# Performance work log

Hardware: AMD Instinct MI355X
Metric: run time of the kernel (lower is better)

Reference implementation:

```python
import jax, jax.numpy as jnp
import numpy as np

S, B, V, E, H = 64, 32, 32000, 512, 1024


def gru_cell(x, h, Wih, Whh, bih, bhh):
    # PyTorch GRU cell math. x: [B, in], h: [B, H]
    gi = x @ Wih.T + bih          # [B, 3H]
    gh = h @ Whh.T + bhh          # [B, 3H]
    ir, iz, inn = jnp.split(gi, 3, axis=-1)
    hr, hz, hn = jnp.split(gh, 3, axis=-1)
    r = jax.nn.sigmoid(ir + hr)
    z = jax.nn.sigmoid(iz + hz)
    n = jnp.tanh(inn + r * hn)
    return (1.0 - z) * n + z * h


def run_gru(xs, h0, Wih, Whh, bih, bhh):
    def step(h, x):
        h = gru_cell(x, h, Wih, Whh, bih, bhh)
        return h, h
    _, hs = jax.lax.scan(step, h0, xs)
    return hs  # [S, B, H]


def setup_inputs():
    key = jax.random.key(0)
    ks = jax.random.split(key, 24)
    n = lambda k, shp, s=0.05: (jax.random.normal(k, shp, jnp.float32) * s)
    inp = {
        "input_seq": jax.random.randint(ks[0], (S, B), 0, V),
        "target_seq": jax.random.randint(ks[1], (S, B), 0, V),
        "emb": n(ks[2], (V, E)),
        # bidirectional encoder GRU (forward / backward directions)
        "enc_Wih_f": n(ks[3], (3 * H, E)), "enc_Whh_f": n(ks[4], (3 * H, H)),
        "enc_bih_f": n(ks[5], (3 * H,)),  "enc_bhh_f": n(ks[6], (3 * H,)),
        "enc_Wih_b": n(ks[7], (3 * H, E)), "enc_Whh_b": n(ks[8], (3 * H, H)),
        "enc_bih_b": n(ks[9], (3 * H,)),  "enc_bhh_b": n(ks[10], (3 * H,)),
        "encoder_init": n(ks[11], (2, H), 0.1),
        # decoder GRU: input = token(E) + glimpse(2H) + last_output(E)
        "dec_Wih": n(ks[12], (3 * H, 2 * E + 2 * H)), "dec_Whh": n(ks[13], (3 * H, H)),
        "dec_bih": n(ks[14], (3 * H,)), "dec_bhh": n(ks[15], (3 * H,)),
        "dec_init_h": n(ks[16], (H,), 0.1),
        "dec_init_out": n(ks[17], (E,), 0.1),
        "attn_W1": n(ks[18], (H, 3 * H)),  # Linear(3H -> H, bias=False)
        "attn_W2": n(ks[19], (1, H)),      # Linear(H -> 1, bias=False)
        "out_W": n(ks[20], (V, H)), "out_b": n(ks[21], (V,)),
    }
    return inp


def reference(input_seq, target_seq, emb,
              enc_Wih_f, enc_Whh_f, enc_bih_f, enc_bhh_f,
              enc_Wih_b, enc_Whh_b, enc_bih_b, enc_bhh_b, encoder_init,
              dec_Wih, dec_Whh, dec_bih, dec_bhh, dec_init_h, dec_init_out,
              attn_W1, attn_W2, out_W, out_b):
    x = emb[input_seq]            # [S, B, E]
    tgt = emb[target_seq]         # [S, B, E]
    bsz = x.shape[1]

    # bidirectional encoder
    h0f = jnp.broadcast_to(encoder_init[0], (bsz, H))
    h0b = jnp.broadcast_to(encoder_init[1], (bsz, H))
    fwd = run_gru(x, h0f, enc_Wih_f, enc_Whh_f, enc_bih_f, enc_bhh_f)
    bwd = run_gru(x[::-1], h0b, enc_Wih_b, enc_Whh_b, enc_bih_b, enc_bhh_b)[::-1]
    enc = jnp.concatenate([fwd, bwd], axis=-1)  # [S, B, 2H]

    def step(carry, inp_t):
        h, last_out = carry                      # [B,H], [B,E]
        tok, tg = inp_t                          # [B,E], [B,E]
        hexp = jnp.broadcast_to(h[None], (S, bsz, H))
        a = jnp.concatenate([enc, hexp], axis=-1)            # [S, B, 3H]
        scores = jnp.tanh(a @ attn_W1.T) @ attn_W2.T          # [S, B, 1]
        # NOTE: original uses nn.Softmax(dim=1) on [S,B,1] -> softmax over BATCH dim
        w = jax.nn.softmax(scores, axis=1)
        glimpse = (enc * w).sum(axis=0)                       # [B, 2H]
        dec_in = jnp.concatenate([tok, glimpse, last_out], axis=-1)
        h = gru_cell(dec_in, h, dec_Wih, dec_Whh, dec_bih, dec_bhh)
        probs = jax.nn.softmax(h @ out_W.T + out_b, axis=1)   # [B, V]
        return (h, tg), probs

    h0 = jnp.broadcast_to(dec_init_h, (bsz, H))
    o0 = jnp.broadcast_to(dec_init_out, (bsz, E))
    _, outs = jax.lax.scan(step, (h0, o0), (x, tgt))
    return outs  # [S, B, V]
```

## Files before the change

kernel.cpp:

```cpp
#include <hip/hip_runtime.h>
#include <hip/hip_bf16.h>

#define S_ 64
#define B_ 32
#define V_ 32000
#define E_ 512
#define H_ 1024
#define H3_ 3072

typedef __hip_bfloat16 bf16;
typedef __attribute__((ext_vector_type(8))) short s8v;
typedef __attribute__((ext_vector_type(4))) float f4;
typedef unsigned long long ull;

__device__ __forceinline__ float b2f(bf16 x){ return __bfloat162float(x); }
__device__ __forceinline__ bf16  f2b(float x){ return __float2bfloat16(x); }
__device__ __forceinline__ float bfu2f(unsigned short u){
  union { unsigned u; float f; } c; c.u = ((unsigned)u) << 16; return c.f;
}
#define MFMA16(a,b,c) __builtin_amdgcn_mfma_f32_16x16x32_bf16((a),(b),(c),0,0,0)

__device__ __forceinline__ float fsigmoid(float x){ return 1.f/(1.f + __expf(-x)); }
__device__ __forceinline__ float ftanh(float x){ float e2 = __expf(2.f*x); return 1.f - 2.f/(e2 + 1.f); }

__global__ __launch_bounds__(256) void cast_bf16_k(const float* __restrict__ s, bf16* __restrict__ d, int n8){
  int stride = gridDim.x*256;
  for (int i = blockIdx.x*256 + threadIdx.x; i < n8; i += stride){
    f4 a = *((const f4*)s + (size_t)i*2);
    f4 b = *((const f4*)s + (size_t)i*2 + 1);
    union { s8v v; bf16 h[8]; } o;
    #pragma unroll
    for (int k=0;k<4;k++){ o.h[k]=f2b(a[k]); o.h[4+k]=f2b(b[k]); }
    *((s8v*)d + i) = o.v;
  }
}
__global__ __launch_bounds__(256) void cast2_k(const float* __restrict__ s0, const float* __restrict__ s1,
                                               bf16* __restrict__ d0, bf16* __restrict__ d1, int n8){
  const float* s = blockIdx.y ? s1 : s0;
  bf16* d = blockIdx.y ? d1 : d0;
  int stride = gridDim.x*256;
  for (int i = blockIdx.x*256 + threadIdx.x; i < n8; i += stride){
    f4 a = *((const f4*)s + (size_t)i*2);
    f4 b = *((const f4*)s + (size_t)i*2 + 1);
    union { s8v v; bf16 h[8]; } o;
    #pragma unroll
    for (int k=0;k<4;k++){ o.h[k]=f2b(a[k]); o.h[4+k]=f2b(b[k]); }
    *((s8v*)d + i) = o.v;
  }
}
__global__ __launch_bounds__(256) void cast4_k(const float* __restrict__ s0, const float* __restrict__ s1,
                                               const float* __restrict__ s2, const float* __restrict__ s3,
                                               bf16* __restrict__ d0, bf16* __restrict__ d1,
                                               bf16* __restrict__ d2, bf16* __restrict__ d3, int n8){
  const float* s = (blockIdx.y==0)?s0:(blockIdx.y==1)?s1:(blockIdx.y==2)?s2:s3;
  bf16* d = (blockIdx.y==0)?d0:(blockIdx.y==1)?d1:(blockIdx.y==2)?d2:d3;
  int stride = gridDim.x*256;
  for (int i = blockIdx.x*256 + threadIdx.x; i < n8; i += stride){
    f4 a = *((const f4*)s + (size_t)i*2);
    f4 b = *((const f4*)s + (size_t)i*2 + 1);
    union { s8v v; bf16 h[8]; } o;
    #pragma unroll
    for (int k=0;k<4;k++){ o.h[k]=f2b(a[k]); o.h[4+k]=f2b(b[k]); }
    *((s8v*)d + i) = o.v;
  }
}
__global__ __launch_bounds__(256) void gather_x_k(const float* __restrict__ emb, const int* __restrict__ seq, bf16* __restrict__ d){
  int i = blockIdx.x*256 + threadIdx.x;
  int row = i >> 6, e8 = i & 63;
  const float* src = emb + (size_t)seq[row]*E_;
  f4 a = *((const f4*)src + e8*2);
  f4 b = *((const f4*)src + e8*2 + 1);
  union { s8v v; bf16 h[8]; } o;
  #pragma unroll
  for (int k=0;k<4;k++){ o.h[k]=f2b(a[k]); o.h[4+k]=f2b(b[k]); }
  *((s8v*)d + i) = o.v;
}
__global__ __launch_bounds__(256) void gather_lo_k(const float* __restrict__ emb, const int* __restrict__ tseq, const float* __restrict__ o0, bf16* __restrict__ d){
  int i = blockIdx.x*256 + threadIdx.x;
  int row = i >> 6, e8 = i & 63;
  int t = row >> 5, b = row & 31;
  const float* src = (t == 0) ? o0 : (emb + (size_t)tseq[(t-1)*B_ + b]*E_);
  f4 a = *((const f4*)src + e8*2);
  f4 c = *((const f4*)src + e8*2 + 1);
  union { s8v v; bf16 h[8]; } o;
  #pragma unroll
  for (int k=0;k<4;k++){ o.h[k]=f2b(a[k]); o.h[4+k]=f2b(c[k]); }
  *((s8v*)d + i) = o.v;
}

template<int WB16, int ACC>
__global__ __launch_bounds__(256) void gemm_bt(const bf16* __restrict__ A, int lda,
                                               const bf16* __restrict__ B, int ldb,
                                               const float* __restrict__ bias,
                                               void* __restrict__ Cp, int ldc, int K)
{
  __shared__ bf16 a_sm[128][40];
  __shared__ bf16 b_sm[128][40];
  const int tid = threadIdx.x;
  const int m0 = blockIdx.y*128, n0 = blockIdx.x*128;
  const int w = tid>>6, l = tid&63;
  const int wm = w>>1, wn = w&1;
  f4 acc[4][4];
  #pragma unroll
  for (int i=0;i<4;i++)
    #pragma unroll
    for (int j=0;j<4;j++) acc[i][j] = (f4){0.f,0.f,0.f,0.f};
  const int srow = tid>>1, skc = (tid&1)*16;
  const int ar = l&15, koff = (l>>4)*8;
  for (int k0 = 0; k0 < K; k0 += 32){
    __syncthreads();
    const s8v* pa = (const s8v*)(A + (size_t)(m0+srow)*lda + k0 + skc);
    const s8v* pb = (const s8v*)(B + (size_t)(n0+srow)*ldb + k0 + skc);
    *(s8v*)&a_sm[srow][skc]   = pa[0];
    *(s8v*)&a_sm[srow][skc+8] = pa[1];
    *(s8v*)&b_sm[srow][skc]   = pb[0];
    *(s8v*)&b_sm[srow][skc+8] = pb[1];
    __syncthreads();
    s8v av[4], bv[4];
    #pragma unroll
    for (int i=0;i<4;i++) av[i] = *(const s8v*)&a_sm[wm*64 + i*16 + ar][koff];
    #pragma unroll
    for (int j=0;j<4;j++) bv[j] = *(const s8v*)&b_sm[wn*64 + j*16 + ar][koff];
    #pragma unroll
    for (int i=0;i<4;i++)
      #pragma unroll
      for (int j=0;j<4;j++)
        acc[i][j] = MFMA16(av[i], bv[j], acc[i][j]);
  }
  const int rb = (l>>4)*4;
  #pragma unroll
  for (int i=0;i<4;i++){
    #pragma unroll
    for (int j=0;j<4;j++){
      int col = n0 + wn*64 + j*16 + ar;
      float badd = bias ? bias[col] : 0.f;
      #pragma unroll
      for (int r=0;r<4;r++){
        int row = m0 + wm*64 + i*16 + rb + r;
        size_t idx = (size_t)row*ldc + col;
        float v = acc[i][j][r] + badd;
        if (ACC) v += ((const float*)Cp)[idx];
        if (WB16) ((bf16*)Cp)[idx] = f2b(v);
        else      ((float*)Cp)[idx] = v;
      }
    }
  }
}

__global__ __launch_bounds__(256) void enc_init_k(const float* __restrict__ enc_init,
                                                  const float* __restrict__ bihf, const float* __restrict__ bihb,
                                                  bf16* __restrict__ hb0, float* __restrict__ hfE,
                                                  float* __restrict__ bias_fb){
  int i = blockIdx.x*256 + threadIdx.x;
  int base = i*8;
  int dir = base>>15, rem = base&32767, col = rem&1023;
  const float* sp = enc_init + dir*H_ + col;
  f4 a = *(const f4*)sp, b = *(const f4*)(sp+4);
  union { s8v v; bf16 h[8]; } o;
  #pragma unroll
  for (int k=0;k<4;k++){ o.h[k]=f2b(a[k]); o.h[4+k]=f2b(b[k]); }
  *(s8v*)(hb0 + dir*32768 + rem) = o.v;
  *(f4*)(hfE + dir*32768 + rem) = a;
  *(f4*)(hfE + dir*32768 + rem + 4) = b;
  if (i < 6144) bias_fb[i] = (i < 3072) ? bihf[i] : bihb[i-3072];
}
__global__ __launch_bounds__(256) void dec_init_k(const float* __restrict__ dinh,
                                                  bf16* __restrict__ hd0, float* __restrict__ hfD){
  int i = blockIdx.x*256 + threadIdx.x;
  int base = i*8;
  int col = base&1023;
  const float* sp = dinh + col;
  f4 a = *(const f4*)sp, b = *(const f4*)(sp+4);
  union { s8v v; bf16 h[8]; } o;
  #pragma unroll
  for (int k=0;k<4;k++){ o.h[k]=f2b(a[k]); o.h[4+k]=f2b(b[k]); }
  *(s8v*)(hd0 + base) = o.v;
  *(f4*)(hfD + base) = a;
  *(f4*)(hfD + base + 4) = b;
}

__global__ __launch_bounds__(256) void enc_step_k(
  const float* __restrict__ gi_fb,
  const bf16* __restrict__ whhf, const bf16* __restrict__ whhb,
  const float* __restrict__ bhhf, const float* __restrict__ bhhb,
  const bf16* __restrict__ hrd_base, bf16* __restrict__ hwr_base,
  float* __restrict__ hfE, bf16* __restrict__ enc_out, int s)
{
  __shared__ bf16 hst[16][1032];
  __shared__ bf16 hsT[16][64];
  const int tid = threadIdx.x, bid = blockIdx.x;
  const int w = tid>>6, l = tid&63;
  const int lr = l&15, koff = (l>>4)*8, rb = (l>>4)*4;
  const int x = bid&7, g3 = bid>>3;
  const int dir = x>>2;
  const int mt = g3>>2;
  const int jtb = (x&3)*16 + (g3&3)*4;
  const int jt = jtb + w;
  const int col = jt*16 + lr;
  const bf16* W    = dir ? whhb : whhf;
  const float* bhh = dir ? bhhb : bhhf;
  const float br_ = bhh[col], bz_ = bhh[H_+col], bn_ = bhh[2*H_+col];
  const bf16* pr = W + (size_t)(jt*16 + lr)*H_ + koff;
  const bf16* pz = pr + (size_t)H_*H_;
  const bf16* pn = pz + (size_t)H_*H_;
  {
    const bf16* src = hrd_base + dir*32768 + (size_t)mt*16*H_;
    #pragma unroll
    for (int c = 0; c < 8; ++c){
      int g = c*256 + tid;
      int row = g>>7, off = g&127;
      *(s8v*)&hst[row][off*8] = *(const s8v*)(src + (size_t)row*H_ + off*8);
    }
  }
  __syncthreads();
  f4 accr = (f4){0,0,0,0}, accz = (f4){0,0,0,0}, accn = (f4){0,0,0,0};
  #pragma unroll 4
  for (int k0 = 0; k0 < H_; k0 += 32){
    s8v a = *(const s8v*)&hst[lr][koff + k0];
    accr = MFMA16(a, *(const s8v*)(pr + k0), accr);
    accz = MFMA16(a, *(const s8v*)(pz + k0), accz);
    accn = MFMA16(a, *(const s8v*)(pn + k0), accn);
  }
  const int es = dir ? (63 - s) : s;
  const int dcol = dir*3072 + col;
  #pragma unroll
  for (int ri = 0; ri < 4; ++ri){
    const int b_ = mt*16 + rb + ri;
    const size_t gr = (size_t)(es*B_ + b_)*6144;
    float ir = gi_fb[gr + dcol], iz = gi_fb[gr + 1024 + dcol], inn = gi_fb[gr + 2048 + dcol];
    float rg = fsigmoid(ir + accr[ri] + br_);
    float zg = fsigmoid(iz + accz[ri] + bz_);
    float ng = ftanh(inn + rg*(accn[ri] + bn_));
    float hold = hfE[dir*32768 + b_*H_ + col];
    float hnew = (1.f - zg)*ng + zg*hold;
    hfE[dir*32768 + b_*H_ + col] = hnew;
    hsT[rb+ri][w*16+lr] = f2b(hnew);
  }
  __syncthreads();
  {
    const int row = tid>>4, seg = tid&15;
    ull v = *(ull*)&hsT[row][seg*4];
    *(ull*)(hwr_base + dir*32768 + (size_t)(mt*16+row)*H_ + jtb*16 + seg*4) = v;
    *(ull*)(enc_out + (size_t)(es*B_ + mt*16+row)*2048 + dir*H_ + jtb*16 + seg*4) = v;
  }
}

__global__ __launch_bounds__(256) void dec_kA(
  const bf16* __restrict__ hd,
  const bf16* __restrict__ whhd, const float* __restrict__ bhhd,
  const bf16* __restrict__ w1b,
  const bf16* __restrict__ encW1b,
  const float* __restrict__ attnW2,
  float* __restrict__ gh,
  float* __restrict__ sc4)
{
  __shared__ bf16 hst[16][1032];
  __shared__ float ghT[16][128];
  __shared__ bf16 hbst[1024];
  __shared__ float hw1s[256];
  const int tid = threadIdx.x, bid = blockIdx.x;
  const int w = tid>>6, l = tid&63;
  const int lr = l&15, koff = (l>>4)*8;
  if (bid < 48){
    const int gmt = bid&1;
    const int rest = bid>>1;
    const int x3 = rest/3, gkk = rest%3;
    const int ntb = x3*24 + gkk*8;
    {
      const bf16* src = hd + (size_t)gmt*16*H_;
      #pragma unroll
      for (int c = 0; c < 8; ++c){
        int g = c*256 + tid;
        int row = g>>7, off = g&127;
        *(s8v*)&hst[row][off*8] = *(const s8v*)(src + (size_t)row*H_ + off*8);
      }
    }
    __syncthreads();
    #pragma unroll
    for (int q = 0; q < 2; ++q){
      const int nt = ntb + w*2 + q;
      const bf16* pb = whhd + (size_t)(nt*16 + lr)*H_ + koff;
      const float bv = bhhd[nt*16 + lr];
      f4 acc = (f4){0,0,0,0};
      #pragma unroll 4
      for (int k0 = 0; k0 < H_; k0 += 32)
        acc = MFMA16(*(const s8v*)&hst[lr][koff+k0], *(const s8v*)(pb+k0), acc);
      #pragma unroll
      for (int r = 0; r < 4; ++r)
        ghT[(l>>4)*4+r][(w*2+q)*16 + lr] = acc[r] + bv;
    }
    __syncthreads();
    #pragma unroll
    for (int i = 0; i < 4; ++i){
      int idx = tid + i*256;
      int row = idx>>6, seg = idx&63;
      union{ float f[2]; ull u; } pk;
      pk.f[0] = ghT[row][seg*2]; pk.f[1] = ghT[row][seg*2+1];
      *(ull*)(gh + (size_t)(gmt*16+row)*H3_ + ntb*16 + seg*2) = pk.u;
    }
  } else {
    const int idx = bid - 48;
    const int b = idx>>2, q = idx&3;
    if (tid < 128) *(s8v*)&hbst[tid*8] = *(const s8v*)(hd + (size_t)b*H_ + tid*8);
    __syncthreads();
    const bf16* pb0 = w1b + (size_t)(q*256 + (w*4+0)*16 + lr)*H3_ + 2048 + koff;
    const bf16* pb1 = w1b + (size_t)(q*256 + (w*4+1)*16 + lr)*H3_ + 2048 + koff;
    const bf16* pb2 = w1b + (size_t)(q*256 + (w*4+2)*16 + lr)*H3_ + 2048 + koff;
    const bf16* pb3 = w1b + (size_t)(q*256 + (w*4+3)*16 + lr)*H3_ + 2048 + koff;
    f4 a0 = (f4){0,0,0,0}, a1 = (f4){0,0,0,0}, a2 = (f4){0,0,0,0}, a3 = (f4){0,0,0,0};
    #pragma unroll 4
    for (int k0 = 0; k0 < H_; k0 += 32){
      s8v a = *(const s8v*)&hbst[koff + k0];
      a0 = MFMA16(a, *(const s8v*)(pb0 + k0), a0);
      a1 = MFMA16(a, *(const s8v*)(pb1 + k0), a1);
      a2 = MFMA16(a, *(const s8v*)(pb2 + k0), a2);
      a3 = MFMA16(a, *(const s8v*)(pb3 + k0), a3);
    }
    if (l < 16){
      hw1s[(w*4+0)*16 + l] = a0[0];
      hw1s[(w*4+1)*16 + l] = a1[0];
      hw1s[(w*4+2)*16 + l] = a2[0];
      hw1s[(w*4+3)*16 + l] = a3[0];
    }
    __syncthreads();
    const int s = tid>>2, part = tid&3;
    const bf16* ep = encW1b + ((size_t)s*B_ + b)*H_ + q*256 + part*64;
    const float* w2p = attnW2 + q*256 + part*64;
    const float* hp = hw1s + part*64;
    float p = 0.f;
    #pragma unroll 2
    for (int ii = 0; ii < 8; ++ii){
      union { s8v v; unsigned short uu[8]; } ev;
      ev.v = *(const s8v*)(ep + ii*8);
      f4 wa = *(const f4*)(w2p + ii*8);
      f4 wb = *(const f4*)(w2p + ii*8 + 4);
      #pragma unroll
      for (int k = 0; k < 8; ++k){
        float xx = bfu2f(ev.uu[k]) + hp[ii*8+k];
        p += (k<4 ? wa[k] : wb[k-4])*ftanh(xx);
      }
    }
    p += __shfl_xor(p,1); p += __shfl_xor(p,2);
    if (part == 0) sc4[q*2048 + s*32 + b] = p;
  }
}

__global__ __launch_bounds__(256) void dec_kB(
  const float* __restrict__ gi_t,
  const bf16* __restrict__ encWgb, const float* __restrict__ gh,
  const float* __restrict__ sc4,
  float* __restrict__ hfD, bf16* __restrict__ hd_w, bf16* __restrict__ hall_t)
{
  __shared__ float watst[64];
  __shared__ float part_[4][3][256];
  __shared__ bf16 hnewst[256];
  const int tid = threadIdx.x, bid = blockIdx.x;
  const int x = bid&7, g3 = bid>>3;
  const int db = 4*x + (g3&3), jq = g3>>2;
  const int jD = jq*256 + tid;
  if (tid < 64){
    const int s = tid;
    f4 v[8];
    #pragma unroll
    for (int c = 0; c < 8; ++c) v[c] = *(const f4*)(sc4 + s*32 + c*4);
    #pragma unroll
    for (int q = 1; q < 4; ++q)
      #pragma unroll
      for (int c = 0; c < 8; ++c) v[c] += *(const f4*)(sc4 + q*2048 + s*32 + c*4);
    float m = -1e30f;
    #pragma unroll
    for (int c = 0; c < 8; ++c)
      #pragma unroll
      for (int k = 0; k < 4; ++k) m = fmaxf(m, v[c][k]);
    float Z = 0.f;
    #pragma unroll
    for (int c = 0; c < 8; ++c)
      #pragma unroll
      for (int k = 0; k < 4; ++k) Z += __expf(v[c][k] - m);
    watst[s] = __expf(v[db>>2][db&3] - m)/Z;
  }
  __syncthreads();
  const int lane = tid&63, wv = tid>>6;
  const int j0 = jq*256 + lane*4;
  f4 g0 = (f4){0,0,0,0}, g1 = (f4){0,0,0,0}, g2 = (f4){0,0,0,0};
  #pragma unroll 4
  for (int i = 0; i < 16; ++i){
    const int s2 = wv*16 + i;
    const float wt = watst[s2];
    const bf16* ro = encWgb + ((size_t)s2*B_ + db)*H3_;
    union{ ull u; unsigned short us[4]; } v0, v1, v2;
    v0.u = *(const ull*)(ro + j0);
    v1.u = *(const ull*)(ro + H_ + j0);
    v2.u = *(const ull*)(ro + 2*H_ + j0);
    #pragma unroll
    for (int k = 0; k < 4; ++k){
      g0[k] += wt*bfu2f(v0.us[k]);
      g1[k] += wt*bfu2f(v1.us[k]);
      g2[k] += wt*bfu2f(v2.us[k]);
    }
  }
  *(f4*)&part_[wv][0][lane*4] = g0;
  *(f4*)&part_[wv][1][lane*4] = g1;
  *(f4*)&part_[wv][2][lane*4] = g2;
  __syncthreads();
  float G0 = part_[0][0][tid]+part_[1][0][tid]+part_[2][0][tid]+part_[3][0][tid];
  float G1 = part_[0][1][tid]+part_[1][1][tid]+part_[2][1][tid]+part_[3][1][tid];
  float G2 = part_[0][2][tid]+part_[1][2][tid]+part_[2][2][tid]+part_[3][2][tid];
  const float* gp = gi_t + (size_t)db*H3_ + jD;
  float ir  = gp[0]    + G0;
  float iz  = gp[H_]   + G1;
  float inn = gp[2*H_] + G2;
  float hr_ = gh[(size_t)db*H3_ + jD];
  float hz_ = gh[(size_t)db*H3_ + H_ + jD];
  float hn_ = gh[(size_t)db*H3_ + 2*H_ + jD];
  float rg = fsigmoid(ir + hr_);
  float zg = fsigmoid(iz + hz_);
  float ng = ftanh(inn + rg*hn_);
  float hold = hfD[(size_t)db*H_ + jD];
  float hnew = (1.f - zg)*ng + zg*hold;
  hfD[(size_t)db*H_ + jD] = hnew;
  hnewst[tid] = f2b(hnew);
  __syncthreads();
  if (tid < 64){
    ull v = *(ull*)&hnewst[tid*4];
    *(ull*)(hd_w + (size_t)db*H_ + jq*256 + tid*4) = v;
    *(ull*)(hall_t + (size_t)db*H_ + jq*256 + tid*4) = v;
  }
}

__global__ __launch_bounds__(256) void softmax_rows_k(float* __restrict__ out){
  __shared__ float wm[4], wl[4];
  const int tid = threadIdx.x;
  float* p = out + (size_t)blockIdx.x*V_;
  float m = -1e30f, lsum = 0.f;
  for (int j = tid; j < V_; j += 256){
    float v = p[j];
    float mn = fmaxf(m, v);
    lsum = lsum*__expf(m - mn) + __expf(v - mn);
    m = mn;
  }
  #pragma unroll
  for (int o = 32; o; o >>= 1){
    float mo = __shfl_xor(m, o), lo_ = __shfl_xor(lsum, o);
    float mn = fmaxf(m, mo);
    lsum = lsum*__expf(m - mn) + lo_*__expf(mo - mn);
    m = mn;
  }
  if ((tid&63)==0){ wm[tid>>6] = m; wl[tid>>6] = lsum; }
  __syncthreads();
  float M = fmaxf(fmaxf(wm[0],wm[1]), fmaxf(wm[2],wm[3]));
  float L = wl[0]*__expf(wm[0]-M) + wl[1]*__expf(wm[1]-M)
          + wl[2]*__expf(wm[2]-M) + wl[3]*__expf(wm[3]-M);
  float inv = 1.f/L;
  for (int j = tid; j < V_; j += 256) p[j] = __expf(p[j]-M)*inv;
}

extern "C" void kernel_launch(void* const* d_in, const int* in_sizes, int n_in,
                              void* d_out, int out_size, void* d_ws, size_t ws_size,
                              hipStream_t stream)
{
  (void)in_sizes; (void)n_in; (void)out_size; (void)ws_size;
  const int*   iseq  = (const int*)d_in[0];
  const int*   tseq  = (const int*)d_in[1];
  const float* emb   = (const float*)d_in[2];
  const float* wihf  = (const float*)d_in[3];
  const float* whhf_f= (const float*)d_in[4];
  const float* bihf  = (const float*)d_in[5];
  const float* bhhf  = (const float*)d_in[6];
  const float* wihb  = (const float*)d_in[7];
  const float* whhb_f= (const float*)d_in[8];
  const float* bihb  = (const float*)d_in[9];
  const float* bhhb  = (const float*)d_in[10];
  const float* einit = (const float*)d_in[11];
  const float* wihd  = (const float*)d_in[12];
  const float* whhd_f= (const float*)d_in[13];
  const float* bihd  = (const float*)d_in[14];
  const float* bhhd  = (const float*)d_in[15];
  const float* dinh  = (const float*)d_in[16];
  const float* dino  = (const float*)d_in[17];
  const float* w1    = (const float*)d_in[18];
  const float* w2    = (const float*)d_in[19];
  const float* outw  = (const float*)d_in[20];
  const float* outb  = (const float*)d_in[21];
  float* out = (float*)d_out;

  char* ws = (char*)d_ws;
  size_t off = 0;
  auto alloc = [&](size_t bytes)->char*{ char* p = ws + off; off += (bytes + 255) & ~(size_t)255; return p; };
  bf16* x_b      = (bf16*)alloc((size_t)2048*512*2);
  bf16* lo_b     = (bf16*)alloc((size_t)2048*512*2);
  bf16* wihf_b   = (bf16*)alloc((size_t)3072*512*2);
  bf16* wihb_b   = (bf16*)alloc((size_t)3072*512*2);
  bf16* whhf_b   = (bf16*)alloc((size_t)3072*1024*2);
  bf16* whhb_b   = (bf16*)alloc((size_t)3072*1024*2);
  bf16* wihd_b   = (bf16*)alloc((size_t)3072*3072*2);
  bf16* whhd_b   = (bf16*)alloc((size_t)3072*1024*2);
  bf16* w1_b     = (bf16*)alloc((size_t)1024*3072*2);
  bf16* outw_b   = (bf16*)alloc((size_t)32000*1024*2);
  float* gi_fb   = (float*)alloc((size_t)2048*6144*4);
  float* gi_d    = (float*)alloc((size_t)2048*3072*4);
  float* bias_fb = (float*)alloc((size_t)6144*4);
  bf16* enc_b    = (bf16*)alloc((size_t)2048*2048*2);
  bf16* encW1_b  = (bf16*)alloc((size_t)2048*1024*2);
  bf16* encWg_b  = (bf16*)alloc((size_t)2048*3072*2);
  bf16*  henc_b  = (bf16*)alloc((size_t)2*65536*2);
  float* hfE     = (float*)alloc((size_t)2*32768*4);
  bf16*  hdb     = (bf16*)alloc((size_t)2*32768*2);
  float* hfD     = (float*)alloc((size_t)32768*4);
  float* ghb     = (float*)alloc((size_t)32*3072*4);
  float* sc4     = (float*)alloc((size_t)4*64*32*4);
  bf16*  hall_b  = (bf16*)alloc((size_t)2048*1024*2);

  gather_x_k <<<512, 256, 0, stream>>>(emb, iseq, x_b);
  gather_lo_k<<<512, 256, 0, stream>>>(emb, tseq, dino, lo_b);
  cast2_k<<<dim3(768,2),  256, 0, stream>>>(wihf, wihb, wihf_b, wihb_b, 196608);
  cast4_k<<<dim3(768,4),  256, 0, stream>>>(whhf_f, whhb_f, whhd_f, w1,
                                            whhf_b, whhb_b, whhd_b, w1_b, 393216);
  cast_bf16_k<<<2048, 256, 0, stream>>>(wihd, wihd_b, 1179648);
  cast_bf16_k<<<2048, 256, 0, stream>>>(outw, outw_b, 4096000);
  enc_init_k<<<32, 256, 0, stream>>>(einit, bihf, bihb, henc_b, hfE, bias_fb);

  gemm_bt<0,0><<<dim3(48,16), 256, 0, stream>>>(x_b, 512, wihf_b,      512,  bias_fb, gi_fb, 6144, 512);
  gemm_bt<0,0><<<dim3(24,16), 256, 0, stream>>>(x_b, 512, wihd_b,      3072, bihd,    gi_d,  3072, 512);
  gemm_bt<0,1><<<dim3(24,16), 256, 0, stream>>>(lo_b,512, wihd_b+2560, 3072, nullptr, gi_d,  3072, 512);

  for (int s = 0; s < 64; ++s){
    const bf16* hrd = henc_b + (size_t)(s&1)*65536;
    bf16*       hwr = henc_b + (size_t)((s+1)&1)*65536;
    enc_step_k<<<64, 256, 0, stream>>>(gi_fb, whhf_b, whhb_b, bhhf, bhhb,
                                       hrd, hwr, hfE, enc_b, s);
  }

  gemm_bt<1,0><<<dim3(8,16),  256, 0, stream>>>(enc_b, 2048, w1_b,       3072, nullptr, encW1_b, 1024, 2048);
  gemm_bt<1,0><<<dim3(24,16), 256, 0, stream>>>(enc_b, 2048, wihd_b+512, 3072, nullptr, encWg_b, 3072, 2048);

  dec_init_k<<<16, 256, 0, stream>>>(dinh, hdb, hfD);
  for (int t = 0; t < 64; ++t){
    const bf16* hdr = hdb + (size_t)(t&1)*32768;
    bf16*       hdw = hdb + (size_t)((t+1)&1)*32768;
    dec_kA<<<176, 256, 0, stream>>>(hdr, whhd_b, bhhd, w1_b, encW1_b, w2, ghb, sc4);
    dec_kB<<<128, 256, 0, stream>>>(gi_d + (size_t)t*B_*H3_, encWg_b, ghb, sc4,
                                    hfD, hdw, hall_b + (size_t)t*B_*H_);
  }

  gemm_bt<0,0><<<dim3(250,16), 256, 0, stream>>>(hall_b, 1024, outw_b, 1024, outb, out, 32000, 1024);
  softmax_rows_k<<<2048, 256, 0, stream>>>(out);
}
```

Baseline: 3.483 ms.

## Fuse softmax partial max/sum into output projection GEMM epilogue with XCD-aware tiling

Replaces the generic output projection GEMM plus a two-pass row softmax with a dedicated GEMM that computes per-tile row max and exp-sum in its epilogue. A small final kernel combines the partial statistics and normalizes the logits in one read-write pass. This removes one full read of the 2048x32000 logits matrix. Block indices are also remapped so consecutive blocks land on different XCDs and grouped tiles improve L2 reuse. The cost is extra shared-memory reductions and aux buffers in the epilogue.

```diff
diff --git a/kernel.cpp b/kernel.cpp
--- a/kernel.cpp
+++ b/kernel.cpp
@@ -144,6 +144,140 @@
         else      ((float*)Cp)[idx] = v;
       }
     }
+  }
+}
+
+__global__ __launch_bounds__(256) void out_gemm_k(
+  const bf16* __restrict__ A, const bf16* __restrict__ Bw,
+  const float* __restrict__ bias, float* __restrict__ C,
+  float* __restrict__ aux_max, float* __restrict__ aux_sum)
+{
+  __shared__ bf16 a_sm[128][40];
+  __shared__ bf16 b_sm[128][40];
+  __shared__ float smax[128][2];
+  __shared__ float ssum[128][2];
+  const int tid = threadIdx.x;
+  const int bid = blockIdx.x;
+  const int xcd = bid & 7, kk = bid >> 3;
+  const int super = kk >> 6, rem = kk & 63;
+  const int sm = super & 1, sn = super >> 1;
+  const int mi = rem & 7, nj = rem >> 3;
+  const int mt = sm*8 + mi, nl = sn*8 + nj;
+  const int nt = nl*8 + xcd;
+  if (nt >= 250) return;
+  const int m0 = mt*128, n0 = nt*128;
+  const int w = tid>>6, l = tid&63;
+  const int wm = w>>1, wn = w&1;
+  f4 acc[4][4];
+  #pragma unroll
+  for (int i=0;i<4;i++)
+    #pragma unroll
+    for (int j=0;j<4;j++) acc[i][j] = (f4){0.f,0.f,0.f,0.f};
+  const int srow = tid>>1, skc = (tid&1)*16;
+  const int ar = l&15, koff = (l>>4)*8;
+  for (int k0 = 0; k0 < 1024; k0 += 32){
+    __syncthreads();
+    const s8v* pa = (const s8v*)(A + (size_t)(m0+srow)*1024 + k0 + skc);
+    const s8v* pb = (const s8v*)(Bw + (size_t)(n0+srow)*1024 + k0 + skc);
+    *(s8v*)&a_sm[srow][skc]   = pa[0];
+    *(s8v*)&a_sm[srow][skc+8] = pa[1];
+    *(s8v*)&b_sm[srow][skc]   = pb[0];
+    *(s8v*)&b_sm[srow][skc+8] = pb[1];
+    __syncthreads();
+    s8v av[4], bv[4];
+    #pragma unroll
+    for (int i=0;i<4;i++) av[i] = *(const s8v*)&a_sm[wm*64 + i*16 + ar][koff];
+    #pragma unroll
+    for (int j=0;j<4;j++) bv[j] = *(const s8v*)&b_sm[wn*64 + j*16 + ar][koff];
+    #pragma unroll
+    for (int i=0;i<4;i++)
+      #pragma unroll
+      for (int j=0;j<4;j++)
+        acc[i][j] = MFMA16(av[i], bv[j], acc[i][j]);
+  }
+  const int rb = (l>>4)*4;
+  float bj[4];
+  #pragma unroll
+  for (int j=0;j<4;j++) bj[j] = bias[n0 + wn*64 + j*16 + ar];
+  float rmax[4][4];
+  #pragma unroll
+  for (int i=0;i<4;i++){
+    #pragma unroll
+    for (int r=0;r<4;r++){
+      float m_ = -1e30f;
+      #pragma unroll
+      for (int j=0;j<4;j++) m_ = fmaxf(m_, acc[i][j][r] + bj[j]);
+      #pragma unroll
+      for (int o=1;o<16;o<<=1) m_ = fmaxf(m_, __shfl_xor(m_, o));
+      rmax[i][r] = m_;
+    }
+  }
+  if ((l&15)==0){
+    #pragma unroll
+    for (int i=0;i<4;i++)
+      #pragma unroll
+      for (int r=0;r<4;r++)
+        smax[wm*64 + i*16 + rb + r][wn] = rmax[i][r];
+  }
+  __syncthreads();
+  #pragma unroll
+  for (int i=0;i<4;i++)
+    #pragma unroll
+    for (int r=0;r<4;r++)
+      rmax[i][r] = fmaxf(smax[wm*64 + i*16 + rb + r][0], smax[wm*64 + i*16 + rb + r][1]);
+  #pragma unroll
+  for (int i=0;i<4;i++){
+    #pragma unroll
+    for (int r=0;r<4;r++){
+      const int row = m0 + wm*64 + i*16 + rb + r;
+      float s_ = 0.f;
+      #pragma unroll
+      for (int j=0;j<4;j++){
+        float v = acc[i][j][r] + bj[j];
+        C[(size_t)row*V_ + n0 + wn*64 + j*16 + ar] = v;
+        s_ += __expf(v - rmax[i][r]);
+      }
+      #pragma unroll
+      for (int o=1;o<16;o<<=1) s_ += __shfl_xor(s_, o);
+      if ((l&15)==0) ssum[wm*64 + i*16 + rb + r][wn] = s_;
+    }
+  }
+  __syncthreads();
+  if (tid < 128){
+    float gm = fmaxf(smax[tid][0], smax[tid][1]);
+    aux_max[(size_t)nt*2048 + m0 + tid] = gm;
+    aux_sum[(size_t)nt*2048 + m0 + tid] = ssum[tid][0] + ssum[tid][1];
+  }
+}
+
+__global__ __launch_bounds__(256) void softmax_final_k(
+  const float* __restrict__ aux_max, const float* __restrict__ aux_sum,
+  float* __restrict__ out)
+{
+  __shared__ float wred[4];
+  const int tid = threadIdx.x;
+  const int row = blockIdx.x;
+  float tm = (tid < 250) ? aux_max[(size_t)tid*2048 + row] : -1e30f;
+  float m = tm;
+  #pragma unroll
+  for (int o=32;o;o>>=1) m = fmaxf(m, __shfl_xor(m,o));
+  if ((tid&63)==0) wred[tid>>6] = m;
+  __syncthreads();
+  float M = fmaxf(fmaxf(wred[0],wred[1]), fmaxf(wred[2],wred[3]));
+  __syncthreads();
+  float ts = (tid < 250) ? aux_sum[(size_t)tid*2048 + row]*__expf(tm - M) : 0.f;
+  #pragma unroll
+  for (int o=32;o;o>>=1) ts += __shfl_xor(ts,o);
+  if ((tid&63)==0) wred[tid>>6] = ts;
+  __syncthreads();
+  float L = wred[0]+wred[1]+wred[2]+wred[3];
+  float inv = 1.f/L;
+  f4* p = (f4*)(out + (size_t)row*V_);
+  for (int j = tid; j < V_/4; j += 256){
+    f4 v = p[j];
+    #pragma unroll
+    for (int k=0;k<4;k++) v[k] = __expf(v[k] - M)*inv;
+    p[j] = v;
   }
 }
 
@@ -426,33 +560,6 @@
     *(ull*)(hd_w + (size_t)db*H_ + jq*256 + tid*4) = v;
     *(ull*)(hall_t + (size_t)db*H_ + jq*256 + tid*4) = v;
   }
-}
-
-__global__ __launch_bounds__(256) void softmax_rows_k(float* __restrict__ out){
-  __shared__ float wm[4], wl[4];
-  const int tid = threadIdx.x;
-  float* p = out + (size_t)blockIdx.x*V_;
-  float m = -1e30f, lsum = 0.f;
-  for (int j = tid; j < V_; j += 256){
-    float v = p[j];
-    float mn = fmaxf(m, v);
-    lsum = lsum*__expf(m - mn) + __expf(v - mn);
-    m = mn;
-  }
-  #pragma unroll
-  for (int o = 32; o; o >>= 1){
-    float mo = __shfl_xor(m, o), lo_ = __shfl_xor(lsum, o);
-    float mn = fmaxf(m, mo);
-    lsum = lsum*__expf(m - mn) + lo_*__expf(mo - mn);
-    m = mn;
-  }
-  if ((tid&63)==0){ wm[tid>>6] = m; wl[tid>>6] = lsum; }
-  __syncthreads();
-  float M = fmaxf(fmaxf(wm[0],wm[1]), fmaxf(wm[2],wm[3]));
-  float L = wl[0]*__expf(wm[0]-M) + wl[1]*__expf(wm[1]-M)
-          + wl[2]*__expf(wm[2]-M) + wl[3]*__expf(wm[3]-M);
-  float inv = 1.f/L;
-  for (int j = tid; j < V_; j += 256) p[j] = __expf(p[j]-M)*inv;
 }
 
 extern "C" void kernel_launch(void* const* d_in, const int* in_sizes, int n_in,
@@ -510,6 +617,8 @@
   float* ghb     = (float*)alloc((size_t)32*3072*4);
   float* sc4     = (float*)alloc((size_t)4*64*32*4);
   bf16*  hall_b  = (bf16*)alloc((size_t)2048*1024*2);
+  float* auxm    = (float*)alloc((size_t)256*2048*4);
+  float* auxs    = (float*)alloc((size_t)256*2048*4);
 
   gather_x_k <<<512, 256, 0, stream>>>(emb, iseq, x_b);
   gather_lo_k<<<512, 256, 0, stream>>>(emb, tseq, dino, lo_b);
@@ -543,6 +652,6 @@
                                     hfD, hdw, hall_b + (size_t)t*B_*H_);
   }
 
-  gemm_bt<0,0><<<dim3(250,16), 256, 0, stream>>>(hall_b, 1024, outw_b, 1024, outb, out, 32000, 1024);
-  softmax_rows_k<<<2048, 256, 0, stream>>>(out);
-}
+  out_gemm_k<<<4096, 256, 0, stream>>>(hall_b, outw_b, outb, out, auxm, auxs);
+  softmax_final_k<<<2048, 256, 0, stream>>>(auxm, auxs, out);
+}
```

Result: no change. 3.434 ms (-1.4%).
